# Kernel optimization log

Measured on AMD Instinct MI355X. Metric: run time of the kernel, lower is better.

The kernel has to match this reference:

```python
import jax, jax.numpy as jnp
import numpy as np
from jax import lax

TEMP = 1e-5
EPS = 1e-20


def _lstm_scan(xs, Wih, Whh, hidden):
    # xs: [S, B, Din]; PyTorch gate order i, f, g, o; no bias
    B = xs.shape[1]
    h0 = jnp.zeros((B, hidden), xs.dtype)
    c0 = jnp.zeros((B, hidden), xs.dtype)

    def step(carry, xt):
        h, c = carry
        g = xt @ Wih.T + h @ Whh.T
        i, f, gg, o = jnp.split(g, 4, axis=-1)
        c = jax.nn.sigmoid(f) * c + jax.nn.sigmoid(i) * jnp.tanh(gg)
        h = jax.nn.sigmoid(o) * jnp.tanh(c)
        return (h, c), h

    _, hs = lax.scan(step, (h0, c0), xs)
    return hs  # [S, B, hidden]


def setup_inputs() -> dict:
    key = jax.random.key(0)
    ks = jax.random.split(key, 16)
    B, S, V, VOCAB, D = 128, 256, 16, 20000, 512
    sc = 0.05
    emb = jax.random.normal(ks[2], (VOCAB + 1, D), jnp.float32) * 0.02
    emb = emb.at[VOCAB].set(0.0)  # padding_idx row
    return {
        "input_seqs": jax.random.randint(ks[0], (B, S, V), 0, VOCAB),
        "mask": jnp.ones((B, S), dtype=bool),
        "lengths": jax.random.randint(ks[1], (B,), 1, S + 1),
        "time_step": jnp.zeros((B, S), dtype=jnp.int32),
        "code_mask": jnp.ones((B, S, V), dtype=bool),
        "emb": emb,
        "rev_Wih": jax.random.normal(ks[3], (40, D), jnp.float32) * sc,
        "rev_Whh": jax.random.normal(ks[4], (40, 10), jnp.float32) * sc,
        "conv_w": jax.random.normal(ks[5], (20, D, 3), jnp.float32) * sc,
        "leap_W1": jax.random.normal(ks[6], (D, 2 * D + 30), jnp.float32) * sc,
        "leap_b1": jnp.zeros((D,), jnp.float32),
        "leap_W2": jax.random.normal(ks[7], (2, D), jnp.float32) * sc,
        "leap_b2": jnp.zeros((2,), jnp.float32),
        "cell_Wih": jax.random.normal(ks[8], (4 * D, D), jnp.float32) * sc,
        "cell_Whh": jax.random.normal(ks[9], (4 * D, D), jnp.float32) * sc,
        "out_W": jax.random.normal(ks[10], (2, D), jnp.float32) * sc,
        "out_b": jnp.zeros((2,), jnp.float32),
    }


def reference(input_seqs, mask, lengths, time_step, code_mask, emb, rev_Wih,
              rev_Whh, conv_w, leap_W1, leap_b1, leap_W2, leap_b2, cell_Wih,
              cell_Whh, out_W, out_b):
    B, S, V = input_seqs.shape
    D = emb.shape[1]
    # embed + sum over codes per visit (dropouts are eval-mode identity)
    x = jnp.take(emb, input_seqs, axis=0).sum(axis=2)  # [B, S, D]

    # reverse LSTM (hidden=10): run on flipped sequence, flip output back
    xs_rev = jnp.flip(x, axis=1).transpose(1, 0, 2)  # [S, B, D]
    back = jnp.flip(_lstm_scan(xs_rev, rev_Wih, rev_Whh, 10).transpose(1, 0, 2), axis=1)  # [B, S, 10]

    # Conv1d(D->20, k=3, pad=1) + ReLU
    cnn = lax.conv_general_dilated(x.transpose(0, 2, 1), conv_w, (1,), ((1, 1),),
                                   dimension_numbers=("NCH", "OIH", "NCH"))
    cnn = jax.nn.relu(cnn).transpose(0, 2, 1)  # [B, S, 20]

    # precomputed gumbel uniforms, one per timestep
    U = jax.random.uniform(jax.random.key(42), (S, B, 2), jnp.float32)

    def step(carry, inp):
        hx, cx = carry
        xt, bt, ct, ut = inp
        feat = jnp.concatenate([hx, xt, bt, ct], axis=-1)  # [B, 2D+30]
        logits = jax.nn.relu(feat @ leap_W1.T + leap_b1) @ leap_W2.T + leap_b2
        logp = jax.nn.log_softmax(logits, axis=-1)
        y = logp - jnp.log(-jnp.log(ut + EPS) + EPS)
        skip = jax.nn.softmax(y / TEMP, axis=-1)  # [B, 2]
        g = xt @ cell_Wih.T + hx @ cell_Whh.T
        i, f, gg, o = jnp.split(g, 4, axis=-1)
        step_cx = jax.nn.sigmoid(f) * cx + jax.nn.sigmoid(i) * jnp.tanh(gg)
        step_hx = jax.nn.sigmoid(o) * jnp.tanh(step_cx)
        hx_new = hx * skip[:, 1:2] + step_hx * skip[:, 0:1]
        return (hx_new, step_cx), hx_new

    h0 = jnp.zeros((B, D), x.dtype)
    c0 = jnp.zeros((B, D), x.dtype)
    xs = (x.transpose(1, 0, 2), back.transpose(1, 0, 2), cnn.transpose(1, 0, 2), U)
    _, hiddens = lax.scan(step, (h0, c0), xs)  # [S, B, D]
    hiddens = hiddens.transpose(1, 0, 2)  # [B, S, D]

    final = hiddens[jnp.arange(B), lengths - 1]  # [B, D]
    out = final @ out_W.T + out_b  # [B, 2]
    return out
```

## Files before the change

### kernel.cpp

```cpp
#include <hip/hip_runtime.h>
#include <math.h>

#define NB 128
#define NS 256
#define ND 512
#define NBS (NB*NS)
#define KE 544
#define NC 2560

typedef unsigned short u16;
typedef __attribute__((ext_vector_type(8))) short s8v;
typedef __attribute__((ext_vector_type(4))) float f4v;
typedef __attribute__((ext_vector_type(4))) unsigned uv4;
typedef __attribute__((ext_vector_type(2))) double dv2;

static constexpr size_t PSA  = (size_t)NBS * KE;
static constexpr size_t PSWE = (size_t)NC  * KE;
static constexpr size_t PSWS = (size_t)NC  * ND;
static constexpr size_t PSH  = (size_t)NB  * ND;

__device__ double g_A[(size_t)NBS * KE];
__device__ u16    g_Ab[3 * PSA];
__device__ float  g_Pre[(size_t)NBS * NC];
__device__ double g_Aproj[(size_t)NBS * 40];
__device__ double g_gum[NS * NB * 2];
__device__ double g_hx[NB * ND];
__device__ u16    g_hxb[3 * NB * ND];
__device__ double g_c[NB * ND];
__device__ float  g_gbufF[NB * NC];
__device__ double g_final[NB * ND];
__device__ float  g_Wext[PSWE];
__device__ u16    g_Wextb[3 * PSWE];
__device__ float  g_Wstep[PSWS];
__device__ u16    g_Wstepb[3 * PSWS];
__device__ double g_lpart[32][NB][2];
__device__ u16    g_hxbG[3 * NB * ND];
__device__ float  g_gbufG[NB * 2048];
__device__ double g_lpartG[32][NB][2];
__device__ int    g_aflag[160 * 32];
__device__ int    g_hxf[NB * 32];
__device__ int    g_ok, g_bad, g_badstep, g_badfused;

__device__ __forceinline__ double sigd(double x) { return 1.0 / (1.0 + exp(-x)); }
__device__ __forceinline__ u16 f2bf(float f) {
    unsigned u = __float_as_uint(f);
    return (u16)((u + 0x7FFFu + ((u >> 16) & 1u)) >> 16);
}
__device__ __forceinline__ float bf2f(u16 b) { return __uint_as_float(((unsigned)b) << 16); }
__device__ __forceinline__ void decomp3(float f, u16& b0, u16& b1, u16& b2) {
    b0 = f2bf(f); float r1 = f - bf2f(b0);
    b1 = f2bf(r1); float r2 = r1 - bf2f(b1);
    b2 = f2bf(r2);
}
__device__ __forceinline__ size_t pre_ix(int m, int n) {
    return ((size_t)(m & 255) * NB + (m >> 8)) * NC + n;
}
__device__ __forceinline__ void put_Ab(size_t ix, float f) {
    u16 b0, b1, b2; decomp3(f, b0, b1, b2);
    g_Ab[ix] = b0; g_Ab[PSA + ix] = b1; g_Ab[2 * PSA + ix] = b2;
}

__device__ __forceinline__ void sc_store_f32(float* p, float v) {
    asm volatile("global_store_dword %0, %1, off sc0 sc1" :: "v"(p), "v"(v) : "memory");
}
__device__ __forceinline__ void sc_store_u16(u16* p, unsigned v) {
    asm volatile("global_store_short %0, %1, off sc0 sc1" :: "v"(p), "v"(v) : "memory");
}
__device__ __forceinline__ void sc_store_u32(void* p, unsigned v) {
    asm volatile("global_store_dword %0, %1, off sc0 sc1" :: "v"(p), "v"(v) : "memory");
}
__device__ __forceinline__ void sc_store_d2(double* p, dv2 v) {
    asm volatile("global_store_dwordx4 %0, %1, off sc0 sc1" :: "v"(p), "v"(v) : "memory");
}
#define SC_WAIT() do { asm volatile("s_waitcnt vmcnt(0)" ::: "memory"); \
                       __builtin_amdgcn_sched_barrier(0); } while (0)

#define MFMA_BF16 __builtin_amdgcn_mfma_f32_16x16x32_bf16
#define STEP6(AP,AC,A0,A1,A2,B0,B1,B2) \
    AP = MFMA_BF16(A0, B0, AP, 0, 0, 0); \
    AC = MFMA_BF16(A0, B1, AC, 0, 0, 0); \
    AC = MFMA_BF16(A1, B0, AC, 0, 0, 0); \
    AC = MFMA_BF16(A0, B2, AC, 0, 0, 0); \
    AC = MFMA_BF16(A1, B1, AC, 0, 0, 0); \
    AC = MFMA_BF16(A2, B0, AC, 0, 0, 0);

__global__ void probe_bf16() {
    int l = threadIdx.x, lr = l & 15, lk = l >> 4;
    s8v a, b;
#pragma unroll
    for (int e = 0; e < 8; ++e) {
        int k = 8 * lk + e;
        a[e] = (short)f2bf((float)(((3 * lr + 7 * k) % 13) + 1));
        b[e] = (short)f2bf((float)(((5 * k + 11 * lr) % 17) + 1));
    }
    f4v d = {0.f, 0.f, 0.f, 0.f};
    d = MFMA_BF16(a, b, d, 0, 0, 0);
    bool okl = true;
#pragma unroll
    for (int r = 0; r < 4; ++r) {
        int row = 4 * lk + r, col = lr;
        int e = 0;
        for (int k = 0; k < 32; ++k)
            e += (((3 * row + 7 * k) % 13) + 1) * (((5 * k + 11 * col) % 17) + 1);
        if (d[r] != (float)e) okl = false;
    }
    unsigned long long vote = __ballot(okl);
    if (l == 0) {
        g_ok = (vote == 0xFFFFFFFFFFFFFFFFull) ? 1 : 0;
        g_bad = 0; g_badstep = 0; g_badfused = 0;
    }
}

__global__ void init_state() {
    int i = blockIdx.x * 256 + threadIdx.x;
    if (i < 160 * 32) g_aflag[i] = 0;
    if (i < NB * 32)  g_hxf[i]  = 0;
    if (i < NB * ND) {
        g_hx[i] = 0.0; g_c[i] = 0.0;
        g_hxb[i] = 0; g_hxb[PSH + i] = 0; g_hxb[2 * PSH + i] = 0;
    }
    if (i < NB * ND / 2) {
#pragma unroll
        for (int p = 0; p < 3; ++p)
            sc_store_u32((void*)(g_hxbG + (size_t)p * PSH + 2 * i), 0u);
    }
}

__global__ __launch_bounds__(256) void build_w(const float* __restrict__ cWih,
                                               const float* __restrict__ cWhh,
                                               const float* __restrict__ W1,
                                               const float* __restrict__ b1) {
    int n = blockIdx.x;
    for (int c = threadIdx.x; c < KE; c += 256) {
        float we;
        if (n < 2048) we = (c < 512) ? cWih[(size_t)n * 512 + c] : 0.f;
        else {
            int n2 = n - 2048;
            if      (c < 512)  we = W1[(size_t)n2 * 1054 + 512 + c];
            else if (c < 522)  we = W1[(size_t)n2 * 1054 + 1024 + (c - 512)];
            else if (c < 542)  we = W1[(size_t)n2 * 1054 + 1034 + (c - 522)];
            else if (c == 542) we = b1[n2];
            else               we = 0.f;
        }
        size_t ix = (size_t)n * KE + c;
        g_Wext[ix] = we;
        u16 b0, b1_, b2; decomp3(we, b0, b1_, b2);
        g_Wextb[ix] = b0; g_Wextb[PSWE + ix] = b1_; g_Wextb[2 * PSWE + ix] = b2;
        if (c < 512) {
            float ws = (n < 2048) ? cWhh[(size_t)n * 512 + c]
                                  : W1[(size_t)(n - 2048) * 1054 + c];
            size_t ix2 = (size_t)n * ND + c;
            g_Wstep[ix2] = ws;
            decomp3(ws, b0, b1_, b2);
            g_Wstepb[ix2] = b0; g_Wstepb[PSWS + ix2] = b1_; g_Wstepb[2 * PSWS + ix2] = b2;
        }
    }
}

__device__ __forceinline__ unsigned rotl32(unsigned x, int r) { return (x << r) | (x >> (32 - r)); }

__global__ void gumbel_init() {
    unsigned p = blockIdx.x * 256 + threadIdx.x;
    if (p >= 65536u) return;
    unsigned k0 = 0u, k1 = 42u;
    unsigned ks2 = k0 ^ k1 ^ 0x1BD11BDAu;
    unsigned x0 = 0u, x1 = p;
    x0 += k0; x1 += k1;
#define RND(r) { x0 += x1; x1 = rotl32(x1, (r)); x1 ^= x0; }
    RND(13) RND(15) RND(26) RND(6)
    x0 += k1;  x1 += ks2 + 1u;
    RND(17) RND(29) RND(16) RND(24)
    x0 += ks2; x1 += k0 + 2u;
    RND(13) RND(15) RND(26) RND(6)
    x0 += k0;  x1 += k1 + 3u;
    RND(17) RND(29) RND(16) RND(24)
    x0 += k1;  x1 += ks2 + 4u;
    RND(13) RND(15) RND(26) RND(6)
    x0 += ks2; x1 += k0 + 5u;
#undef RND
    unsigned bits = x0 ^ x1;
    float u = __uint_as_float((bits >> 9) | 0x3f800000u) - 1.0f;
    g_gum[p] = log(-log((double)u + 1e-20) + 1e-20);
}

__global__ __launch_bounds__(128) void embed_sum(const int* __restrict__ seqs,
                                                 const float* __restrict__ emb) {
    int bs = blockIdx.x;
    int tid = threadIdx.x;
    __shared__ int idxs[16];
    if (tid < 16) idxs[tid] = seqs[(size_t)bs * 16 + tid];
    __syncthreads();
    double a0 = 0, a1 = 0, a2 = 0, a3 = 0;
    for (int v = 0; v < 16; ++v) {
        const float4* row = (const float4*)(emb + (size_t)idxs[v] * ND);
        float4 e = row[tid];
        a0 += (double)e.x; a1 += (double)e.y; a2 += (double)e.z; a3 += (double)e.w;
    }
    size_t base = (size_t)bs * KE + tid * 4;
    double* o = g_A + base;
    o[0] = a0; o[1] = a1; o[2] = a2; o[3] = a3;
    put_Ab(base + 0, (float)a0); put_Ab(base + 1, (float)a1);
    put_Ab(base + 2, (float)a2); put_Ab(base + 3, (float)a3);
    if (tid == 0) {
        g_A[(size_t)bs * KE + 542] = 1.0; g_A[(size_t)bs * KE + 543] = 0.0;
        put_Ab((size_t)bs * KE + 542, 1.0f); put_Ab((size_t)bs * KE + 543, 0.0f);
    }
}

__global__ __launch_bounds__(256) void gemm_f64(
    const double* __restrict__ A, int lda,
    const float* __restrict__ W, int ldw,
    double* __restrict__ C, int ldc,
    int M, int N, int K) {
    __shared__ double As[16][66];
    __shared__ double Ws[16][66];
    int m0 = blockIdx.x * 64, n0 = blockIdx.y * 64;
    int tid = threadIdx.x, tx = tid & 15, ty = tid >> 4;
    double acc[4][4] = {};
    for (int k0 = 0; k0 < K; k0 += 16) {
        for (int i = tid; i < 1024; i += 256) {
            int r = i >> 4, c = i & 15;
            As[c][r] = (m0 + r < M && k0 + c < K) ? A[(size_t)(m0 + r) * lda + k0 + c] : 0.0;
            Ws[c][r] = (n0 + r < N && k0 + c < K) ? (double)W[(size_t)(n0 + r) * ldw + k0 + c] : 0.0;
        }
        __syncthreads();
#pragma unroll
        for (int kk = 0; kk < 16; ++kk) {
            double a0 = As[kk][ty*4], a1 = As[kk][ty*4+1], a2 = As[kk][ty*4+2], a3 = As[kk][ty*4+3];
            double w0 = Ws[kk][tx*4], w1 = Ws[kk][tx*4+1], w2 = Ws[kk][tx*4+2], w3 = Ws[kk][tx*4+3];
            acc[0][0] += a0*w0; acc[0][1] += a0*w1; acc[0][2] += a0*w2; acc[0][3] += a0*w3;
            acc[1][0] += a1*w0; acc[1][1] += a1*w1; acc[1][2] += a1*w2; acc[1][3] += a1*w3;
            acc[2][0] += a2*w0; acc[2][1] += a2*w1; acc[2][2] += a2*w2; acc[2][3] += a2*w3;
            acc[3][0] += a3*w0; acc[3][1] += a3*w1; acc[3][2] += a3*w2; acc[3][3] += a3*w3;
        }
        __syncthreads();
    }
#pragma unroll
    for (int i = 0; i < 4; ++i)
#pragma unroll
        for (int j = 0; j < 4; ++j) {
            int m = m0 + ty*4 + i, n = n0 + tx*4 + j;
            if (m < M && n < N) C[(size_t)m * ldc + n] = acc[i][j];
        }
}

__global__ __launch_bounds__(64) void rev_lstm(const float* __restrict__ Whh) {
    int b = blockIdx.x;
    int tid = threadIdx.x;
    __shared__ double h[10], cc[10], g[40], wsh[400];
    for (int i = tid; i < 400; i += 64) wsh[i] = (double)Whh[i];
    if (tid < 10) { h[tid] = 0.0; cc[tid] = 0.0; }
    __syncthreads();
    for (int s = NS - 1; s >= 0; --s) {
        if (tid < 40) {
            double acc = g_Aproj[((size_t)b * NS + s) * 40 + tid];
#pragma unroll
            for (int k = 0; k < 10; ++k) acc += h[k] * wsh[tid * 10 + k];
            g[tid] = acc;
        }
        __syncthreads();
        if (tid < 10) {
            double gi = g[tid], gf = g[10 + tid], gg = g[20 + tid], go = g[30 + tid];
            double cn = sigd(gf) * cc[tid] + sigd(gi) * tanh(gg);
            cc[tid] = cn;
            double hn = sigd(go) * tanh(cn);
            h[tid] = hn;
            size_t ix = ((size_t)b * NS + s) * KE + 512 + tid;
            g_A[ix] = hn;
            put_Ab(ix, (float)hn);
        }
        __syncthreads();
    }
}

__global__ __launch_bounds__(256) void conv_relu(const float* __restrict__ w) {
    int b = blockIdx.x, s0 = blockIdx.y * 8;
    int tid = threadIdx.x, grp = tid >> 5, lane = tid & 31;
    __shared__ double xs[10][ND];
    for (int i = tid; i < 10 * ND; i += 256) {
        int r = i >> 9, d = i & (ND - 1);
        int s = s0 - 1 + r;
        xs[r][d] = (s >= 0 && s < NS) ? g_A[((size_t)b * NS + s) * KE + d] : 0.0;
    }
    __syncthreads();
    int s = s0 + grp;
    for (int o = 0; o < 20; ++o) {
        const float* wo = w + (size_t)o * 1536;
        double acc = 0.0;
        for (int d = lane; d < ND; d += 32) {
            acc += xs[grp][d]     * (double)wo[d*3]
                 + xs[grp + 1][d] * (double)wo[d*3 + 1]
                 + xs[grp + 2][d] * (double)wo[d*3 + 2];
        }
        for (int m = 16; m > 0; m >>= 1) acc += __shfl_xor(acc, m, 32);
        if (lane == 0) {
            double v = acc > 0.0 ? acc : 0.0;
            size_t ix = ((size_t)b * NS + s) * KE + 522 + o;
            g_A[ix] = v;
            put_Ab(ix, (float)v);
        }
    }
}

__global__ __launch_bounds__(256) void big_gemm() {
    __shared__ __align__(16) unsigned char shms[36864];
    int tid = threadIdx.x;
    int n0 = blockIdx.x * 64, m0 = blockIdx.y * 64;
    if (g_ok) {
        u16* usA = (u16*)shms;
        u16* usB = usA + 9216;
        int lane = tid & 63, wave = tid >> 6;
        int wm = (wave & 1) * 32, wn = (wave >> 1) * 32;
        int lr = lane & 15, lk = lane >> 4;
        f4v z = {0.f,0.f,0.f,0.f};
        f4v aP00=z,aP01=z,aP10=z,aP11=z, aC00=z,aC01=z,aC10=z,aC11=z;
        for (int k0 = 0; k0 < KE; k0 += 32) {
            for (int i = tid; i < 1536; i += 256) {
                if (i < 768) {
                    int p = i >> 8, rem = i & 255, r = rem >> 2, sg = rem & 3;
                    *(uint4*)(void*)(usA + p*3072 + r*48 + sg*8) =
                        *(const uint4*)(const void*)(g_Ab + (size_t)p*PSA + (size_t)(m0+r)*KE + k0 + sg*8);
                } else {
                    int j = i - 768;
                    int p = j >> 8, rem = j & 255, r = rem >> 2, sg = rem & 3;
                    *(uint4*)(void*)(usB + p*3072 + r*48 + sg*8) =
                        *(const uint4*)(const void*)(g_Wextb + (size_t)p*PSWE + (size_t)(n0+r)*KE + k0 + sg*8);
                }
            }
            __syncthreads();
            const u16* pa = usA + (wm + lr) * 48 + 8 * lk;
            const u16* pb = usB + (wn + lr) * 48 + 8 * lk;
            s8v a0_0 = *(const s8v*)(const void*)(pa);
            s8v a0_1 = *(const s8v*)(const void*)(pa + 768);
            s8v a1_0 = *(const s8v*)(const void*)(pa + 3072);
            s8v a1_1 = *(const s8v*)(const void*)(pa + 3840);
            s8v a2_0 = *(const s8v*)(const void*)(pa + 6144);
            s8v a2_1 = *(const s8v*)(const void*)(pa + 6912);
            s8v b0_0 = *(const s8v*)(const void*)(pb);
            s8v b0_1 = *(const s8v*)(const void*)(pb + 768);
            s8v b1_0 = *(const s8v*)(const void*)(pb + 3072);
            s8v b1_1 = *(const s8v*)(const void*)(pb + 3840);
            s8v b2_0 = *(const s8v*)(const void*)(pb + 6144);
            s8v b2_1 = *(const s8v*)(const void*)(pb + 6912);
            STEP6(aP00, aC00, a0_0, a1_0, a2_0, b0_0, b1_0, b2_0)
            STEP6(aP01, aC01, a0_0, a1_0, a2_0, b0_1, b1_1, b2_1)
            STEP6(aP10, aC10, a0_1, a1_1, a2_1, b0_0, b1_0, b2_0)
            STEP6(aP11, aC11, a0_1, a1_1, a2_1, b0_1, b1_1, b2_1)
            __syncthreads();
        }
        int rb = m0 + wm + 4 * lk, cb0 = n0 + wn + lr, cb1 = cb0 + 16;
#pragma unroll
        for (int r = 0; r < 4; ++r) {
            g_Pre[pre_ix(rb + r, cb0)]      = aP00[r] + aC00[r];
            g_Pre[pre_ix(rb + r, cb1)]      = aP01[r] + aC01[r];
            g_Pre[pre_ix(rb + 16 + r, cb0)] = aP10[r] + aC10[r];
            g_Pre[pre_ix(rb + 16 + r, cb1)] = aP11[r] + aC11[r];
        }
    } else {
        double* Asd = (double*)shms;
        double* Wsd = Asd + 64 * 33;
        int tx = tid & 15, ty = tid >> 4;
        double acc[4][4] = {};
        for (int k0 = 0; k0 < KE; k0 += 32) {
            for (int i = tid; i < 2048; i += 256) {
                int r = i >> 5, c = i & 31;
                Asd[r * 33 + c] = g_A[(size_t)(m0 + r) * KE + k0 + c];
                Wsd[r * 33 + c] = (double)g_Wext[(size_t)(n0 + r) * KE + k0 + c];
            }
            __syncthreads();
            for (int kk = 0; kk < 32; ++kk) {
                double a0 = Asd[(ty*4)*33+kk], a1 = Asd[(ty*4+1)*33+kk], a2 = Asd[(ty*4+2)*33+kk], a3 = Asd[(ty*4+3)*33+kk];
                double w0 = Wsd[(tx*4)*33+kk], w1 = Wsd[(tx*4+1)*33+kk], w2 = Wsd[(tx*4+2)*33+kk], w3 = Wsd[(tx*4+3)*33+kk];
                acc[0][0] += a0*w0; acc[0][1] += a0*w1; acc[0][2] += a0*w2; acc[0][3] += a0*w3;
                acc[1][0] += a1*w0; acc[1][1] += a1*w1; acc[1][2] += a1*w2; acc[1][3] += a1*w3;
                acc[2][0] += a2*w0; acc[2][1] += a2*w1; acc[2][2] += a2*w2; acc[2][3] += a2*w3;
                acc[3][0] += a3*w0; acc[3][1] += a3*w1; acc[3][2] += a3*w2; acc[3][3] += a3*w3;
            }
            __syncthreads();
        }
#pragma unroll
        for (int i = 0; i < 4; ++i)
#pragma unroll
            for (int j = 0; j < 4; ++j)
                g_Pre[pre_ix(m0 + ty*4 + i, n0 + tx*4 + j)] = (float)acc[i][j];
    }
}

__global__ void verify_pre() {
    int s = blockIdx.x * 256 + threadIdx.x;
    unsigned m = ((unsigned)s * 2654435761u) & 32767u;
    unsigned n = ((unsigned)s * 40503u + 7u) % 2560u;
    double dot = 0.0;
    const double* ar = g_A + (size_t)m * KE;
    const float*  wr = g_Wext + (size_t)n * KE;
    for (int c = 0; c < KE; ++c) dot += ar[c] * (double)wr[c];
    double got = (double)g_Pre[pre_ix((int)m, (int)n)];
    if (fabs(got - dot) > 1e-4 * (1.0 + fabs(dot))) atomicOr(&g_bad, 1);
}

__global__ __launch_bounds__(256) void big_fix() {
    if (!(g_ok && g_bad)) return;
    __shared__ double As[64][33];
    __shared__ double Ws[64][33];
    int tid = threadIdx.x, tx = tid & 15, ty = tid >> 4;
    for (int tile = blockIdx.x; tile < (NC/64) * (NBS/64); tile += gridDim.x) {
        int n0 = (tile % (NC/64)) * 64, m0 = (tile / (NC/64)) * 64;
        double acc[4][4] = {};
        for (int k0 = 0; k0 < KE; k0 += 32) {
            for (int i = tid; i < 2048; i += 256) {
                int r = i >> 5, c = i & 31;
                As[r][c] = g_A[(size_t)(m0 + r) * KE + k0 + c];
                Ws[r][c] = (double)g_Wext[(size_t)(n0 + r) * KE + k0 + c];
            }
            __syncthreads();
            for (int kk = 0; kk < 32; ++kk) {
                double a0 = As[ty*4][kk], a1 = As[ty*4+1][kk], a2 = As[ty*4+2][kk], a3 = As[ty*4+3][kk];
                double w0 = Ws[tx*4][kk], w1 = Ws[tx*4+1][kk], w2 = Ws[tx*4+2][kk], w3 = Ws[tx*4+3][kk];
                acc[0][0] += a0*w0; acc[0][1] += a0*w1; acc[0][2] += a0*w2; acc[0][3] += a0*w3;
                acc[1][0] += a1*w0; acc[1][1] += a1*w1; acc[1][2] += a1*w2; acc[1][3] += a1*w3;
                acc[2][0] += a2*w0; acc[2][1] += a2*w1; acc[2][2] += a2*w2; acc[2][3] += a2*w3;
                acc[3][0] += a3*w0; acc[3][1] += a3*w1; acc[3][2] += a3*w2; acc[3][3] += a3*w3;
            }
            __syncthreads();
        }
#pragma unroll
        for (int i = 0; i < 4; ++i)
#pragma unroll
            for (int j = 0; j < 4; ++j)
                g_Pre[pre_ix(m0 + ty*4 + i, n0 + tx*4 + j)] = (float)acc[i][j];
        __syncthreads();
    }
}

__global__ void synth_hx() {
    int i = blockIdx.x * 256 + threadIdx.x;
    if (i >= NB * ND) return;
    unsigned h = (unsigned)i * 2654435761u;
    float v = (float)((h >> 8) & 0xFFFFu) / 65536.0f - 0.5f;
    g_hx[i] = (double)v;
    u16 b0, b1, b2; decomp3(v, b0, b1, b2);
    g_hxb[i] = b0; g_hxb[PSH + i] = b1; g_hxb[2 * PSH + i] = b2;
    sc_store_u16(g_hxbG + i, b0);
    sc_store_u16(g_hxbG + PSH + i, b1);
    sc_store_u16(g_hxbG + 2 * PSH + i, b2);
}

__global__ __launch_bounds__(256) void step_gemm(int t, int probe) {
    __shared__ double shd[3168];
    int tid = threadIdx.x;
    int m0 = blockIdx.x * 32, n0 = blockIdx.y * 64;
    int use_mfma = g_ok && (probe || !g_badstep);
    if (use_mfma) {
        int lane = tid & 63, wave = tid >> 6;
        int wm = (wave & 1) * 16, wn = (wave >> 1) * 32;
        int lr = lane & 15, lk = lane >> 4;
        size_t ha  = (size_t)(m0 + wm + lr) * ND;
        size_t wb0 = (size_t)(n0 + wn + lr) * ND;
        size_t wb1 = (size_t)(n0 + wn + 16 + lr) * ND;
        f4v z = {0.f,0.f,0.f,0.f};
        f4v aP0=z, aP1=z, aC0=z, aC1=z;
        for (int k0 = 0; k0 < ND; k0 += 32) {
            int kk = k0 + 8 * lk;
            s8v a0  = *(const s8v*)(const void*)(g_hxb + ha + kk);
            s8v a1  = *(const s8v*)(const void*)(g_hxb + PSH + ha + kk);
            s8v a2  = *(const s8v*)(const void*)(g_hxb + 2*PSH + ha + kk);
            s8v b00 = *(const s8v*)(const void*)(g_Wstepb + wb0 + kk);
            s8v b01 = *(const s8v*)(const void*)(g_Wstepb + wb1 + kk);
            s8v b10 = *(const s8v*)(const void*)(g_Wstepb + PSWS + wb0 + kk);
            s8v b11 = *(const s8v*)(const void*)(g_Wstepb + PSWS + wb1 + kk);
            s8v b20 = *(const s8v*)(const void*)(g_Wstepb + 2*PSWS + wb0 + kk);
            s8v b21 = *(const s8v*)(const void*)(g_Wstepb + 2*PSWS + wb1 + kk);
            STEP6(aP0, aC0, a0, a1, a2, b00, b10, b20)
            STEP6(aP1, aC1, a0, a1, a2, b01, b11, b21)
        }
        int rb = m0 + wm + 4 * lk, cb0 = n0 + wn + lr, cb1 = cb0 + 16;
#pragma unroll
        for (int r = 0; r < 4; ++r) {
            g_gbufF[(size_t)(rb + r) * NC + cb0] = aP0[r] + aC0[r]
                + g_Pre[((size_t)t * NB + rb + r) * NC + cb0];
            g_gbufF[(size_t)(rb + r) * NC + cb1] = aP1[r] + aC1[r]
                + g_Pre[((size_t)t * NB + rb + r) * NC + cb1];
        }
    } else {
        double* Asd = shd;
        double* Wsd = shd + 1056;
        int tx = tid & 15, ty = tid >> 4;
        double acc[2][4] = {};
        for (int k0 = 0; k0 < ND; k0 += 32) {
            for (int i = tid; i < 1024; i += 256) {
                int r = i >> 5, c = i & 31;
                Asd[r * 33 + c] = g_hx[(size_t)(m0 + r) * ND + k0 + c];
            }
            for (int i = tid; i < 2048; i += 256) {
                int r = i >> 5, c = i & 31;
                Wsd[r * 33 + c] = (double)g_Wstep[(size_t)(n0 + r) * ND + k0 + c];
            }
            __syncthreads();
            for (int kk = 0; kk < 32; ++kk) {
                double a0 = Asd[(ty*2)*33+kk], a1 = Asd[(ty*2+1)*33+kk];
                double w0 = Wsd[(tx*4)*33+kk], w1 = Wsd[(tx*4+1)*33+kk], w2 = Wsd[(tx*4+2)*33+kk], w3 = Wsd[(tx*4+3)*33+kk];
                acc[0][0] += a0*w0; acc[0][1] += a0*w1; acc[0][2] += a0*w2; acc[0][3] += a0*w3;
                acc[1][0] += a1*w0; acc[1][1] += a1*w1; acc[1][2] += a1*w2; acc[1][3] += a1*w3;
            }
            __syncthreads();
        }
#pragma unroll
        for (int i = 0; i < 2; ++i)
#pragma unroll
            for (int j = 0; j < 4; ++j) {
                int m = m0 + ty*2 + i, n = n0 + tx*4 + j;
                g_gbufF[(size_t)m * NC + n] = (float)(acc[i][j]
                    + (double)g_Pre[((size_t)t * NB + m) * NC + n]);
            }
    }
}

__global__ void verify_step() {
    int s = blockIdx.x * 256 + threadIdx.x;
    unsigned m = ((unsigned)s * 2654435761u) & 127u;
    unsigned n = ((unsigned)s * 40503u + 7u) % 2560u;
    double dot = 0.0;
    const double* hr = g_hx + (size_t)m * ND;
    const float*  wr = g_Wstep + (size_t)n * ND;
    for (int c = 0; c < ND; ++c) dot += hr[c] * (double)wr[c];
    dot += (double)g_Pre[(size_t)m * NC + n];
    double got = (double)g_gbufF[(size_t)m * NC + n];
    if (fabs(got - dot) > 1e-4 * (1.0 + fabs(dot))) atomicOr(&g_badstep, 1);
}

__global__ void verify_fused(const float* __restrict__ W2) {
    int s = blockIdx.x * 256 + threadIdx.x;
    unsigned m = ((unsigned)s * 2654435761u) & 127u;
    unsigned h2 = (unsigned)s * 40503u + 7u;
    const double* hr = g_hx + (size_t)m * ND;
    if (s & 1) {
        unsigned q = h2 & 31u;
        double p0 = 0.0, p1 = 0.0;
        for (int c = 0; c < 16; ++c) {
            int col = q * 16 + c;
            const float* wr = g_Wstep + (size_t)(2048 + col) * ND;
            double dot = 0.0;
            for (int k = 0; k < ND; ++k) dot += hr[k] * (double)wr[k];
            dot += (double)g_Pre[(size_t)m * NC + 2048 + col];
            double hh = dot > 0.0 ? dot : 0.0;
            p0 += hh * (double)W2[col];
            p1 += hh * (double)W2[512 + col];
        }
        if (fabs(g_lpartG[q][m][0] - p0) > 1e-4 * (1.0 + fabs(p0)) ||
            fabs(g_lpartG[q][m][1] - p1) > 1e-4 * (1.0 + fabs(p1)))
            atomicOr(&g_badfused, 1);
    } else {
        unsigned n = h2 % 2048u;
        double dot = 0.0;
        const float* wr = g_Wstep + (size_t)n * ND;
        for (int k = 0; k < ND; ++k) dot += hr[k] * (double)wr[k];
        dot += (double)g_Pre[(size_t)m * NC + n];
        double got = (double)g_gbufG[(size_t)m * 2048 + n];
        if (fabs(got - dot) > 1e-4 * (1.0 + fabs(dot))) atomicOr(&g_badfused, 1);
    }
}

__global__ __launch_bounds__(256) void step_update(
    const float* __restrict__ W2, const float* __restrict__ b2,
    const int* __restrict__ lengths, int t) {
    __shared__ double red[8];
    __shared__ double skipsh[2];
    int b = blockIdx.x, tid = threadIdx.x, lane = tid & 63, wave = tid >> 6;
    const float* gb = g_gbufF + (size_t)b * NC;
    double p0 = 0.0, p1 = 0.0;
    for (int j = tid; j < ND; j += 256) {
        double h = (double)gb[2048 + j];
        h = h > 0.0 ? h : 0.0;
        p0 += h * (double)W2[j];
        p1 += h * (double)W2[ND + j];
    }
    for (int off = 32; off > 0; off >>= 1) {
        p0 += __shfl_down(p0, off, 64);
        p1 += __shfl_down(p1, off, 64);
    }
    if (lane == 0) { red[wave*2] = p0; red[wave*2+1] = p1; }
    __syncthreads();
    if (tid == 0) {
        double l0 = red[0]+red[2]+red[4]+red[6] + (double)b2[0];
        double l1 = red[1]+red[3]+red[5]+red[7] + (double)b2[1];
        double mx = fmax(l0, l1);
        double sh0 = l0 - mx, sh1 = l1 - mx;
        double lsum = log(exp(sh0) + exp(sh1));
        double y0 = (sh0 - lsum) - g_gum[(size_t)t * (NB * 2) + b * 2 + 0];
        double y1 = (sh1 - lsum) - g_gum[(size_t)t * (NB * 2) + b * 2 + 1];
        double xx0 = y0 / 1e-5, xx1 = y1 / 1e-5;
        double mm = fmax(xx0, xx1);
        double e0 = exp(xx0 - mm), e1 = exp(xx1 - mm);
        double inv = 1.0 / (e0 + e1);
        skipsh[0] = e0 * inv; skipsh[1] = e1 * inv;
    }
    __syncthreads();
    double s0 = skipsh[0], s1 = skipsh[1];
    bool isFinal = (t == lengths[b] - 1);
#pragma unroll
    for (int e = 0; e < 2; ++e) {
        int j = tid + 256 * e;
        size_t ix = (size_t)b * ND + j;
        double gi = (double)gb[j], gf = (double)gb[ND + j];
        double gg = (double)gb[2*ND + j], go = (double)gb[3*ND + j];
        double cn = sigd(gf) * g_c[ix] + sigd(gi) * tanh(gg);
        double shx = sigd(go) * tanh(cn);
        double hn = g_hx[ix] * s1 + shx * s0;
        g_c[ix] = cn; g_hx[ix] = hn;
        u16 w0, w1, w2x; decomp3((float)hn, w0, w1, w2x);
        g_hxb[ix] = w0; g_hxb[PSH + ix] = w1; g_hxb[2 * PSH + ix] = w2x;
        if (isFinal) g_final[ix] = hn;
    }
}

__global__ __launch_bounds__(512, 1) void loop_fused(const float* __restrict__ W2,
                                                     const float* __restrict__ b2,
                                                     const int* __restrict__ lengths,
                                                     int steps, int probe) {
    __shared__ __align__(16) unsigned char shm[53504];
    int bid = blockIdx.x, tid = threadIdx.x;
    int nc0 = bid * 16;
    int w = tid >> 6, lane = tid & 63;
    int lr = lane & 15, lk = lane >> 4;
    int path = g_ok && !g_badfused;
    double c0 = 0.0, h0 = 0.0;
    int mylen = (bid < NB) ? lengths[bid] : -1;
    u16*    Wl     = (u16*)shm;
    float*  Wfb    = (float*)shm;
    float*  W2l    = (float*)(shm + 49152);
    double* skipsh = (double*)(shm + 53248);
    if (path) {
        for (int i = tid; i < 3072; i += 512) {
            int p = i >> 10, rem = i & 1023, kk = rem >> 6, l = rem & 63;
            int col = l & 15, k8 = l >> 4;
            *(uint4*)(void*)(Wl + (size_t)p*8192 + kk*512 + l*8) =
                *(const uint4*)(const void*)(g_Wstepb + (size_t)p*PSWS
                      + (size_t)(nc0 + col)*ND + kk*32 + k8*8);
        }
    } else {
        for (int i = tid; i < 16*512; i += 512)
            Wfb[(i >> 9)*521 + (i & 511)] = g_Wstep[(size_t)(nc0 + (i >> 9))*ND + (i & 511)];
    }
    for (int i = tid; i < 1024; i += 512) W2l[i] = W2[i];
    __syncthreads();
    int r0 = 16*w + 4*lk;
    float preA[4];
    if (path) {
#pragma unroll
        for (int r = 0; r < 4; ++r)
            preA[r] = g_Pre[((size_t)0 * NB + r0 + r) * NC + nc0 + lr];
    }
    for (int t = 0; t < steps; ++t) {
        if (path) {
            if (t > 0) {
                for (;;) {
                    bool ok = true;
                    if (lane < 16)
                        ok = (__hip_atomic_load(&g_hxf[(16*w + lane)*32],
                               __ATOMIC_RELAXED, __HIP_MEMORY_SCOPE_AGENT) >= t);
                    if (__all(ok)) break;
                    __builtin_amdgcn_s_sleep(1);
                }
            }
            f4v z = {0.f,0.f,0.f,0.f};
            f4v aP = z, aC = z;
            size_t ha = (size_t)(16*w + lr) * ND;
#pragma unroll
            for (int h = 0; h < 2; ++h) {
                uv4 U0[8], U1[8], U2[8];
#pragma unroll
                for (int kk = 0; kk < 8; ++kk) {
                    int kb = (8*h + kk)*32 + 8*lk;
                    const u16* p0 = g_hxbG + ha + kb;
                    const u16* p1 = g_hxbG + PSH + ha + kb;
                    const u16* p2 = g_hxbG + 2*PSH + ha + kb;
                    asm volatile("global_load_dwordx4 %0, %3, off sc0 sc1\n\t"
                                 "global_load_dwordx4 %1, %4, off sc0 sc1\n\t"
                                 "global_load_dwordx4 %2, %5, off sc0 sc1"
                                 : "=v"(U0[kk]), "=v"(U1[kk]), "=v"(U2[kk])
                                 : "v"(p0), "v"(p1), "v"(p2));
                }
                SC_WAIT();
#pragma unroll
                for (int kk = 0; kk < 8; ++kk) {
                    const u16* wp = Wl + (8*h + kk)*512 + lane*8;
                    s8v B0 = *(const s8v*)(const void*)(wp);
                    s8v B1 = *(const s8v*)(const void*)(wp + 8192);
                    s8v B2 = *(const s8v*)(const void*)(wp + 16384);
                    s8v A0 = __builtin_bit_cast(s8v, U0[kk]);
                    s8v A1 = __builtin_bit_cast(s8v, U1[kk]);
                    s8v A2 = __builtin_bit_cast(s8v, U2[kk]);
                    STEP6(aP, aC, A0, A1, A2, B0, B1, B2)
                }
            }
            if (bid < NB) {
#pragma unroll
                for (int r = 0; r < 4; ++r) {
                    float v = aP[r] + aC[r] + preA[r];
                    sc_store_f32(g_gbufG + (size_t)(r0 + r) * 2048 + nc0 + lr, v);
                }
            } else {
                int colg = nc0 - 2048 + lr;
                double q0[4], q1[4];
#pragma unroll
                for (int r = 0; r < 4; ++r) {
                    float v = aP[r] + aC[r] + preA[r];
                    double hh = v > 0.f ? (double)v : 0.0;
                    q0[r] = hh * (double)W2l[colg];
                    q1[r] = hh * (double)W2l[512 + colg];
                }
#pragma unroll
                for (int m = 8; m > 0; m >>= 1)
#pragma unroll
                    for (int r = 0; r < 4; ++r) {
                        q0[r] += __shfl_xor(q0[r], m, 16);
                        q1[r] += __shfl_xor(q1[r], m, 16);
                    }
                if (lr == 0) {
#pragma unroll
                    for (int r = 0; r < 4; ++r) {
                        dv2 q; q[0] = q0[r]; q[1] = q1[r];
                        sc_store_d2(&g_lpartG[bid - NB][r0 + r][0], q);
                    }
                }
            }
            asm volatile("s_waitcnt vmcnt(0)" ::: "memory");
            __syncthreads();
            if (tid == 0)
                __hip_atomic_store(&g_aflag[bid*32], t + 1, __ATOMIC_RELAXED,
                                   __HIP_MEMORY_SCOPE_AGENT);
            __syncthreads();
            {
                int tn = (t + 1 < steps) ? t + 1 : t;
#pragma unroll
                for (int r = 0; r < 4; ++r)
                    preA[r] = g_Pre[((size_t)tn * NB + r0 + r) * NC + nc0 + lr];
            }
            if (!probe && bid < NB) {
                if (tid < 160) {
                    while (__hip_atomic_load(&g_aflag[tid*32], __ATOMIC_RELAXED,
                             __HIP_MEMORY_SCOPE_AGENT) < t + 1)
                        __builtin_amdgcn_s_sleep(1);
                }
                __syncthreads();
                float gi_f, gf_f, gg_f, go_f;
                {
                    const float* gp = g_gbufG + (size_t)bid * 2048 + tid;
                    asm volatile("global_load_dword %0, %4, off sc0 sc1\n\t"
                                 "global_load_dword %1, %5, off sc0 sc1\n\t"
                                 "global_load_dword %2, %6, off sc0 sc1\n\t"
                                 "global_load_dword %3, %7, off sc0 sc1"
                                 : "=v"(gi_f), "=v"(gf_f), "=v"(gg_f), "=v"(go_f)
                                 : "v"(gp), "v"(gp + 512), "v"(gp + 1024), "v"(gp + 1536));
                }
                double p0 = 0.0, p1 = 0.0;
                if (tid < 32) {
                    dv2 lp;
                    const double* lpp = &g_lpartG[tid][bid][0];
                    asm volatile("global_load_dwordx4 %0, %1, off sc0 sc1"
                                 : "=v"(lp) : "v"(lpp));
                    asm volatile("s_waitcnt vmcnt(0)" ::: "memory");
                    p0 = lp[0]; p1 = lp[1];
                }
                __builtin_amdgcn_sched_barrier(0);
                if (tid < 64) {
#pragma unroll
                    for (int m = 16; m > 0; m >>= 1) {
                        p0 += __shfl_xor(p0, m, 32);
                        p1 += __shfl_xor(p1, m, 32);
                    }
                }
                if (tid == 0) {
                    double l0 = p0 + (double)b2[0], l1 = p1 + (double)b2[1];
                    double mx = fmax(l0, l1);
                    double sh0 = l0 - mx, sh1 = l1 - mx;
                    double lsum = log(exp(sh0) + exp(sh1));
                    double y0 = (sh0 - lsum) - g_gum[(size_t)t * (NB*2) + bid*2 + 0];
                    double y1 = (sh1 - lsum) - g_gum[(size_t)t * (NB*2) + bid*2 + 1];
                    double xx0 = y0 / 1e-5, xx1 = y1 / 1e-5;
                    double mm = fmax(xx0, xx1);
                    double e0 = exp(xx0 - mm), e1 = exp(xx1 - mm);
                    double inv = 1.0 / (e0 + e1);
                    skipsh[0] = e0 * inv; skipsh[1] = e1 * inv;
                }
                __syncthreads();
                SC_WAIT();
                double s0 = skipsh[0], s1 = skipsh[1];
                bool isFinal = (t == mylen - 1);
                size_t ix = (size_t)bid * ND + tid;
                double gi = (double)gi_f, gf = (double)gf_f;
                double gg = (double)gg_f, go = (double)go_f;
                double cn = sigd(gf) * c0 + sigd(gi) * tanh(gg);
                double shx = sigd(go) * tanh(cn);
                double hn = h0 * s1 + shx * s0;
                c0 = cn; h0 = hn;
                u16 w0_, w1_, w2_; decomp3((float)hn, w0_, w1_, w2_);
                sc_store_u16(g_hxbG + ix, w0_);
                sc_store_u16(g_hxbG + PSH + ix, w1_);
                sc_store_u16(g_hxbG + 2*PSH + ix, w2_);
                if (isFinal) g_final[ix] = hn;
                asm volatile("s_waitcnt vmcnt(0)" ::: "memory");
                __syncthreads();
                if (tid == 0)
                    __hip_atomic_store(&g_hxf[bid*32], t + 1, __ATOMIC_RELAXED,
                                       __HIP_MEMORY_SCOPE_AGENT);
            }
        } else {
            if (t > 0) {
                if (tid < NB) {
                    while (__hip_atomic_load(&g_hxf[tid*32], __ATOMIC_RELAXED,
                             __HIP_MEMORY_SCOPE_AGENT) < t)
                        __builtin_amdgcn_s_sleep(1);
                }
                __syncthreads();
                if (tid == 0) __builtin_amdgcn_fence(__ATOMIC_ACQUIRE, "agent");
                __syncthreads();
            }
            int col = tid & 15, rgrp = tid >> 4;
            double q0[4] = {}, q1[4] = {};
#pragma unroll
            for (int rr = 0; rr < 4; ++rr) {
                int row = rgrp*4 + rr;
                const double* hr = g_hx + (size_t)row * ND;
                double dot = 0.0;
                for (int k = 0; k < ND; ++k) dot += hr[k] * (double)Wfb[col*521 + k];
                float v = (float)(dot + (double)g_Pre[((size_t)t * NB + row) * NC + nc0 + col]);
                if (bid < NB) {
                    g_gbufF[(size_t)row * 2048 + nc0 + col] = v;
                } else {
                    double hh = v > 0.f ? (double)v : 0.0;
                    q0[rr] = hh * (double)W2l[nc0 - 2048 + col];
                    q1[rr] = hh * (double)W2l[512 + nc0 - 2048 + col];
                }
            }
            if (bid >= NB) {
#pragma unroll
                for (int m = 8; m > 0; m >>= 1)
#pragma unroll
                    for (int rr = 0; rr < 4; ++rr) {
                        q0[rr] += __shfl_xor(q0[rr], m, 16);
                        q1[rr] += __shfl_xor(q1[rr], m, 16);
                    }
                if (col == 0)
#pragma unroll
                    for (int rr = 0; rr < 4; ++rr) {
                        g_lpart[bid - NB][rgrp*4 + rr][0] = q0[rr];
                        g_lpart[bid - NB][rgrp*4 + rr][1] = q1[rr];
                    }
            }
            __syncthreads();
            if (tid == 0) {
                __builtin_amdgcn_fence(__ATOMIC_RELEASE, "agent");
                __hip_atomic_store(&g_aflag[bid*32], t + 1, __ATOMIC_RELAXED,
                                   __HIP_MEMORY_SCOPE_AGENT);
            }
            __syncthreads();
            if (!probe && bid < NB) {
                if (tid < 160) {
                    while (__hip_atomic_load(&g_aflag[tid*32], __ATOMIC_RELAXED,
                             __HIP_MEMORY_SCOPE_AGENT) < t + 1)
                        __builtin_amdgcn_s_sleep(1);
                }
                __syncthreads();
                if (tid == 0) __builtin_amdgcn_fence(__ATOMIC_ACQUIRE, "agent");
                __syncthreads();
                double p0 = 0.0, p1 = 0.0;
                if (tid < 32) { p0 = g_lpart[tid][bid][0]; p1 = g_lpart[tid][bid][1]; }
                if (tid < 64) {
#pragma unroll
                    for (int m = 16; m > 0; m >>= 1) {
                        p0 += __shfl_xor(p0, m, 32);
                        p1 += __shfl_xor(p1, m, 32);
                    }
                }
                if (tid == 0) {
                    double l0 = p0 + (double)b2[0], l1 = p1 + (double)b2[1];
                    double mx = fmax(l0, l1);
                    double sh0 = l0 - mx, sh1 = l1 - mx;
                    double lsum = log(exp(sh0) + exp(sh1));
                    double y0 = (sh0 - lsum) - g_gum[(size_t)t * (NB*2) + bid*2 + 0];
                    double y1 = (sh1 - lsum) - g_gum[(size_t)t * (NB*2) + bid*2 + 1];
                    double xx0 = y0 / 1e-5, xx1 = y1 / 1e-5;
                    double mm = fmax(xx0, xx1);
                    double e0 = exp(xx0 - mm), e1 = exp(xx1 - mm);
                    double inv = 1.0 / (e0 + e1);
                    skipsh[0] = e0 * inv; skipsh[1] = e1 * inv;
                }
                __syncthreads();
                double s0 = skipsh[0], s1 = skipsh[1];
                bool isFinal = (t == mylen - 1);
                int j = tid;
                size_t ix = (size_t)bid * ND + j;
                const float* gb = g_gbufF + (size_t)bid * 2048;
                double gi = (double)gb[j], gf = (double)gb[512 + j];
                double gg = (double)gb[1024 + j], go = (double)gb[1536 + j];
                double cn = sigd(gf) * c0 + sigd(gi) * tanh(gg);
                double shx = sigd(go) * tanh(cn);
                double hn = h0 * s1 + shx * s0;
                c0 = cn; h0 = hn;
                g_hx[ix] = hn;
                if (isFinal) g_final[ix] = hn;
                __syncthreads();
                if (tid == 0) {
                    __builtin_amdgcn_fence(__ATOMIC_RELEASE, "agent");
                    __hip_atomic_store(&g_hxf[bid*32], t + 1, __ATOMIC_RELAXED,
                                       __HIP_MEMORY_SCOPE_AGENT);
                }
            }
        }
    }
}

__global__ __launch_bounds__(256) void final_out(const float* __restrict__ Wo,
                                                 const float* __restrict__ bo,
                                                 float* __restrict__ out) {
    int tid = threadIdx.x;
    int b = tid >> 1, k = tid & 1;
    double acc = 0.0;
    const double* f = g_final + (size_t)b * ND;
    const float* w = Wo + (size_t)k * ND;
    for (int d = 0; d < ND; ++d) acc += f[d] * (double)w[d];
    out[b * 2 + k] = (float)(acc + (double)bo[k]);
}

extern "C" void kernel_launch(void* const* d_in, const int* in_sizes, int n_in,
                              void* d_out, int out_size, void* d_ws, size_t ws_size,
                              hipStream_t stream) {
    (void)in_sizes; (void)n_in; (void)d_ws; (void)ws_size; (void)out_size;
    const int*   seqs    = (const int*)d_in[0];
    const int*   lengths = (const int*)d_in[2];
    const float* emb     = (const float*)d_in[5];
    const float* revWih  = (const float*)d_in[6];
    const float* revWhh  = (const float*)d_in[7];
    const float* convw   = (const float*)d_in[8];
    const float* W1      = (const float*)d_in[9];
    const float* b1      = (const float*)d_in[10];
    const float* W2      = (const float*)d_in[11];
    const float* b2      = (const float*)d_in[12];
    const float* cWih    = (const float*)d_in[13];
    const float* cWhh    = (const float*)d_in[14];
    const float* Wo      = (const float*)d_in[15];
    const float* bo      = (const float*)d_in[16];
    float* out = (float*)d_out;

    double *A_p = nullptr, *Ap_p = nullptr;
    hipGetSymbolAddress((void**)&A_p,  HIP_SYMBOL(g_A));
    hipGetSymbolAddress((void**)&Ap_p, HIP_SYMBOL(g_Aproj));

    probe_bf16<<<1, 64, 0, stream>>>();
    build_w<<<NC, 256, 0, stream>>>(cWih, cWhh, W1, b1);
    gumbel_init<<<256, 256, 0, stream>>>();
    embed_sum<<<NBS, 128, 0, stream>>>(seqs, emb);

    gemm_f64<<<dim3(NBS / 64, 1), 256, 0, stream>>>(A_p, KE, revWih, ND, Ap_p, 40,
                                                    NBS, 40, ND);
    rev_lstm<<<NB, 64, 0, stream>>>(revWhh);
    conv_relu<<<dim3(NB, NS / 8), 256, 0, stream>>>(convw);

    big_gemm<<<dim3(NC / 64, NBS / 64), 256, 0, stream>>>();
    verify_pre<<<32, 256, 0, stream>>>();
    big_fix<<<2048, 256, 0, stream>>>();

    synth_hx<<<256, 256, 0, stream>>>();
    step_gemm<<<dim3(4, 40), 256, 0, stream>>>(0, 1);
    verify_step<<<8, 256, 0, stream>>>();
    {
        int steps1 = 1, probe1 = 1;
        void* pargs[] = { (void*)&W2, (void*)&b2, (void*)&lengths,
                          (void*)&steps1, (void*)&probe1 };
        hipError_t pe = hipLaunchCooperativeKernel((const void*)loop_fused,
                                                   dim3(160), dim3(512), pargs, 0, stream);
        if (pe == hipSuccess) verify_fused<<<16, 256, 0, stream>>>(W2);
        else (void)hipGetLastError();
    }
    init_state<<<256, 256, 0, stream>>>();

    int stepsN = NS, probe0 = 0;
    void* args[] = { (void*)&W2, (void*)&b2, (void*)&lengths,
                     (void*)&stepsN, (void*)&probe0 };
    hipError_t ce = hipLaunchCooperativeKernel((const void*)loop_fused,
                                               dim3(160), dim3(512), args, 0, stream);
    if (ce != hipSuccess) {
        (void)hipGetLastError();
        for (int t = 0; t < NS; ++t) {
            step_gemm<<<dim3(4, 40), 256, 0, stream>>>(t, 0);
            step_update<<<NB, 256, 0, stream>>>(W2, b2, lengths, t);
        }
    }
    final_out<<<1, 256, 0, stream>>>(Wo, bo, out);
}
```

Before: 9.082 ms.

## Enlarge big_gemm tiles to 128x128 with 4x4 MFMA fragments per wave

The precompute GEMM tile grows from 64x64 to 128x128 per block. Each wave now holds a 4x4 grid of 16x16 accumulators and reuses A and B fragments across them, which raises arithmetic intensity and cuts redundant global and LDS loads. The LDS row stride changes from 48 to 40 elements, and the bf16x3 split MFMA order is merged into a single accumulator. This raises register and LDS use and may lower occupancy. The fp64 fallback path loops over four 64x64 subtiles to match the new grid.

Result: faster. 8.889 ms (-2.1%).

```diff
diff --git a/kernel.cpp b/kernel.cpp
--- a/kernel.cpp
+++ b/kernel.cpp
@@ -303,86 +303,96 @@
 }
 
 __global__ __launch_bounds__(256) void big_gemm() {
-    __shared__ __align__(16) unsigned char shms[36864];
+    __shared__ __align__(16) unsigned char shms[61440];
     int tid = threadIdx.x;
-    int n0 = blockIdx.x * 64, m0 = blockIdx.y * 64;
+    int n0 = blockIdx.x * 128, m0 = blockIdx.y * 128;
     if (g_ok) {
         u16* usA = (u16*)shms;
-        u16* usB = usA + 9216;
+        u16* usB = usA + 15360;
         int lane = tid & 63, wave = tid >> 6;
-        int wm = (wave & 1) * 32, wn = (wave >> 1) * 32;
+        int wm = (wave & 1) * 64, wn = (wave >> 1) * 64;
         int lr = lane & 15, lk = lane >> 4;
-        f4v z = {0.f,0.f,0.f,0.f};
-        f4v aP00=z,aP01=z,aP10=z,aP11=z, aC00=z,aC01=z,aC10=z,aC11=z;
+        f4v acc[4][4];
+#pragma unroll
+        for (int i = 0; i < 4; ++i)
+#pragma unroll
+            for (int j = 0; j < 4; ++j) { f4v z = {0.f,0.f,0.f,0.f}; acc[i][j] = z; }
         for (int k0 = 0; k0 < KE; k0 += 32) {
-            for (int i = tid; i < 1536; i += 256) {
-                if (i < 768) {
-                    int p = i >> 8, rem = i & 255, r = rem >> 2, sg = rem & 3;
-                    *(uint4*)(void*)(usA + p*3072 + r*48 + sg*8) =
-                        *(const uint4*)(const void*)(g_Ab + (size_t)p*PSA + (size_t)(m0+r)*KE + k0 + sg*8);
-                } else {
-                    int j = i - 768;
-                    int p = j >> 8, rem = j & 255, r = rem >> 2, sg = rem & 3;
-                    *(uint4*)(void*)(usB + p*3072 + r*48 + sg*8) =
-                        *(const uint4*)(const void*)(g_Wextb + (size_t)p*PSWE + (size_t)(n0+r)*KE + k0 + sg*8);
-                }
+            for (int i = tid; i < 3072; i += 256) {
+                int isB = i >= 1536, ii = i - isB * 1536;
+                int p = ii >> 9, rem = ii & 511, r = rem >> 2, sg = rem & 3;
+                const u16* src = (isB ? g_Wextb + (size_t)p*PSWE + (size_t)(n0 + r)*KE
+                                      : g_Ab   + (size_t)p*PSA  + (size_t)(m0 + r)*KE)
+                                 + k0 + sg*8;
+                u16* dst = (isB ? usB : usA) + p*5120 + r*40 + sg*8;
+                *(uint4*)(void*)dst = *(const uint4*)(const void*)src;
             }
             __syncthreads();
-            const u16* pa = usA + (wm + lr) * 48 + 8 * lk;
-            const u16* pb = usB + (wn + lr) * 48 + 8 * lk;
-            s8v a0_0 = *(const s8v*)(const void*)(pa);
-            s8v a0_1 = *(const s8v*)(const void*)(pa + 768);
-            s8v a1_0 = *(const s8v*)(const void*)(pa + 3072);
-            s8v a1_1 = *(const s8v*)(const void*)(pa + 3840);
-            s8v a2_0 = *(const s8v*)(const void*)(pa + 6144);
-            s8v a2_1 = *(const s8v*)(const void*)(pa + 6912);
-            s8v b0_0 = *(const s8v*)(const void*)(pb);
-            s8v b0_1 = *(const s8v*)(const void*)(pb + 768);
-            s8v b1_0 = *(const s8v*)(const void*)(pb + 3072);
-            s8v b1_1 = *(const s8v*)(const void*)(pb + 3840);
-            s8v b2_0 = *(const s8v*)(const void*)(pb + 6144);
-            s8v b2_1 = *(const s8v*)(const void*)(pb + 6912);
-            STEP6(aP00, aC00, a0_0, a1_0, a2_0, b0_0, b1_0, b2_0)
-            STEP6(aP01, aC01, a0_0, a1_0, a2_0, b0_1, b1_1, b2_1)
-            STEP6(aP10, aC10, a0_1, a1_1, a2_1, b0_0, b1_0, b2_0)
-            STEP6(aP11, aC11, a0_1, a1_1, a2_1, b0_1, b1_1, b2_1)
+            s8v Af[4][3];
+#pragma unroll
+            for (int fr = 0; fr < 4; ++fr)
+#pragma unroll
+                for (int p = 0; p < 3; ++p)
+                    Af[fr][p] = *(const s8v*)(const void*)(usA + p*5120 + (wm + fr*16 + lr)*40 + 8*lk);
+#pragma unroll
+            for (int fc = 0; fc < 4; ++fc) {
+                s8v B0 = *(const s8v*)(const void*)(usB + 0*5120 + (wn + fc*16 + lr)*40 + 8*lk);
+                s8v B1 = *(const s8v*)(const void*)(usB + 1*5120 + (wn + fc*16 + lr)*40 + 8*lk);
+                s8v B2 = *(const s8v*)(const void*)(usB + 2*5120 + (wn + fc*16 + lr)*40 + 8*lk);
+#pragma unroll
+                for (int fr = 0; fr < 4; ++fr) {
+                    f4v a = acc[fr][fc];
+                    a = MFMA_BF16(Af[fr][0], B0, a, 0, 0, 0);
+                    a = MFMA_BF16(Af[fr][0], B1, a, 0, 0, 0);
+                    a = MFMA_BF16(Af[fr][1], B0, a, 0, 0, 0);
+                    a = MFMA_BF16(Af[fr][0], B2, a, 0, 0, 0);
+                    a = MFMA_BF16(Af[fr][1], B1, a, 0, 0, 0);
+                    a = MFMA_BF16(Af[fr][2], B0, a, 0, 0, 0);
+                    acc[fr][fc] = a;
+                }
+            }
             __syncthreads();
         }
-        int rb = m0 + wm + 4 * lk, cb0 = n0 + wn + lr, cb1 = cb0 + 16;
-#pragma unroll
-        for (int r = 0; r < 4; ++r) {
-            g_Pre[pre_ix(rb + r, cb0)]      = aP00[r] + aC00[r];
-            g_Pre[pre_ix(rb + r, cb1)]      = aP01[r] + aC01[r];
-            g_Pre[pre_ix(rb + 16 + r, cb0)] = aP10[r] + aC10[r];
-            g_Pre[pre_ix(rb + 16 + r, cb1)] = aP11[r] + aC11[r];
-        }
+#pragma unroll
+        for (int fr = 0; fr < 4; ++fr)
+#pragma unroll
+            for (int fc = 0; fc < 4; ++fc)
+#pragma unroll
+                for (int r = 0; r < 4; ++r)
+                    g_Pre[pre_ix(m0 + wm + fr*16 + 4*lk + r, n0 + wn + fc*16 + lr)]
+                        = acc[fr][fc][r];
     } else {
         double* Asd = (double*)shms;
         double* Wsd = Asd + 64 * 33;
         int tx = tid & 15, ty = tid >> 4;
-        double acc[4][4] = {};
-        for (int k0 = 0; k0 < KE; k0 += 32) {
-            for (int i = tid; i < 2048; i += 256) {
-                int r = i >> 5, c = i & 31;
-                Asd[r * 33 + c] = g_A[(size_t)(m0 + r) * KE + k0 + c];
-                Wsd[r * 33 + c] = (double)g_Wext[(size_t)(n0 + r) * KE + k0 + c];
-            }
+        for (int qm = 0; qm < 2; ++qm)
+        for (int qn = 0; qn < 2; ++qn) {
+            int mq = m0 + qm * 64, nq = n0 + qn * 64;
+            double acc[4][4] = {};
+            for (int k0 = 0; k0 < KE; k0 += 32) {
+                for (int i = tid; i < 2048; i += 256) {
+                    int r = i >> 5, c = i & 31;
+                    Asd[r * 33 + c] = g_A[(size_t)(mq + r) * KE + k0 + c];
+                    Wsd[r * 33 + c] = (double)g_Wext[(size_t)(nq + r) * KE + k0 + c];
+                }
+                __syncthreads();
+                for (int kk = 0; kk < 32; ++kk) {
+                    double a0 = Asd[(ty*4)*33+kk], a1 = Asd[(ty*4+1)*33+kk], a2 = Asd[(ty*4+2)*33+kk], a3 = Asd[(ty*4+3)*33+kk];
+                    double w0 = Wsd[(tx*4)*33+kk], w1 = Wsd[(tx*4+1)*33+kk], w2 = Wsd[(tx*4+2)*33+kk], w3 = Wsd[(tx*4+3)*33+kk];
+                    acc[0][0] += a0*w0; acc[0][1] += a0*w1; acc[0][2] += a0*w2; acc[0][3] += a0*w3;
+                    acc[1][0] += a1*w0; acc[1][1] += a1*w1; acc[1][2] += a1*w2; acc[1][3] += a1*w3;
+                    acc[2][0] += a2*w0; acc[2][1] += a2*w1; acc[2][2] += a2*w2; acc[2][3] += a2*w3;
+                    acc[3][0] += a3*w0; acc[3][1] += a3*w1; acc[3][2] += a3*w2; acc[3][3] += a3*w3;
+                }
+                __syncthreads();
+            }
+#pragma unroll
+            for (int i = 0; i < 4; ++i)
+#pragma unroll
+                for (int j = 0; j < 4; ++j)
+                    g_Pre[pre_ix(mq + ty*4 + i, nq + tx*4 + j)] = (float)acc[i][j];
             __syncthreads();
-            for (int kk = 0; kk < 32; ++kk) {
-                double a0 = Asd[(ty*4)*33+kk], a1 = Asd[(ty*4+1)*33+kk], a2 = Asd[(ty*4+2)*33+kk], a3 = Asd[(ty*4+3)*33+kk];
-                double w0 = Wsd[(tx*4)*33+kk], w1 = Wsd[(tx*4+1)*33+kk], w2 = Wsd[(tx*4+2)*33+kk], w3 = Wsd[(tx*4+3)*33+kk];
-                acc[0][0] += a0*w0; acc[0][1] += a0*w1; acc[0][2] += a0*w2; acc[0][3] += a0*w3;
-                acc[1][0] += a1*w0; acc[1][1] += a1*w1; acc[1][2] += a1*w2; acc[1][3] += a1*w3;
-                acc[2][0] += a2*w0; acc[2][1] += a2*w1; acc[2][2] += a2*w2; acc[2][3] += a2*w3;
-                acc[3][0] += a3*w0; acc[3][1] += a3*w1; acc[3][2] += a3*w2; acc[3][3] += a3*w3;
-            }
-            __syncthreads();
-        }
-#pragma unroll
-        for (int i = 0; i < 4; ++i)
-#pragma unroll
-            for (int j = 0; j < 4; ++j)
-                g_Pre[pre_ix(m0 + ty*4 + i, n0 + tx*4 + j)] = (float)acc[i][j];
+        }
     }
 }
 
@@ -957,7 +967,7 @@
     rev_lstm<<<NB, 64, 0, stream>>>(revWhh);
     conv_relu<<<dim3(NB, NS / 8), 256, 0, stream>>>(convw);
 
-    big_gemm<<<dim3(NC / 64, NBS / 64), 256, 0, stream>>>();
+    big_gemm<<<dim3(NC / 128, NBS / 128), 256, 0, stream>>>();
     verify_pre<<<32, 256, 0, stream>>>();
     big_fix<<<2048, 256, 0, stream>>>();
 
```
